# Kernel tuning notes

Hardware: AMD Instinct MI355X
Metric: run time of the kernel (lower is better)

## Reference

```python
import jax, jax.numpy as jnp
from jax import lax
import numpy as np

B = 16384
EPS = 1e-5


def conv2d(x, w, b, pad):
    # x: [N,C,H,W], w: [O,I,kh,kw]
    y = lax.conv_general_dilated(x, w, (1, 1), [(pad, pad), (pad, pad)],
                                 dimension_numbers=("NCHW", "OIHW", "NCHW"))
    return y + b[None, :, None, None]


def maxpool2(x):
    return lax.reduce_window(x, -jnp.inf, lax.max, (1, 1, 2, 2), (1, 1, 2, 2), "VALID")


def setup_inputs() -> dict:
    key = jax.random.key(0)
    ks = jax.random.split(key, 16)
    n = jax.random.normal
    return {
        "x": n(ks[0], (B, 1, 28, 28), dtype=jnp.float32),
        "conv1_w": n(ks[1], (8, 1, 3, 3), dtype=jnp.float32) * 0.2,
        "conv1_b": n(ks[2], (8,), dtype=jnp.float32) * 0.1,
        "conv2_w": n(ks[3], (16, 8, 3, 3), dtype=jnp.float32) * 0.1,
        "conv2_b": n(ks[4], (16,), dtype=jnp.float32) * 0.1,
        "s1_w": n(ks[5], (4, 2), dtype=jnp.float32) * 0.5,
        "s1_b": n(ks[6], (4,), dtype=jnp.float32) * 0.1,
        "s2_w": n(ks[7], (2, 4), dtype=jnp.float32) * 0.5,
        "s2_b": n(ks[8], (2,), dtype=jnp.float32) * 0.1,
        "filt_w": n(ks[9], (1, 1, 2, 2), dtype=jnp.float32) * 0.5,
        "filt_b": n(ks[10], (1,), dtype=jnp.float32) * 0.1,
        "fc1_w": n(ks[11], (64, 787), dtype=jnp.float32) * 0.03,
        "fc1_b": n(ks[12], (64,), dtype=jnp.float32) * 0.1,
        "fc2_w": n(ks[13], (4, 64), dtype=jnp.float32) * 0.1,
        "fc2_b": n(ks[14], (4,), dtype=jnp.float32) * 0.1,
        "bn_g": jnp.ones((4,), dtype=jnp.float32),
        "bn_b": jnp.zeros((4,), dtype=jnp.float32),
    }


def reference(x, conv1_w, conv1_b, conv2_w, conv2_b, s1_w, s1_b, s2_w, s2_b,
              filt_w, filt_b, fc1_w, fc1_b, fc2_w, fc2_b, bn_g, bn_b):
    bsz = x.shape[0]
    # feature extractor: conv3x3 -> relu -> maxpool2 (x2)
    f = maxpool2(jax.nn.relu(conv2d(x, conv1_w, conv1_b, 1)))        # [B,8,14,14]
    f = maxpool2(jax.nn.relu(conv2d(f, conv2_w, conv2_b, 1)))        # [B,16,7,7]
    flat = f.reshape(bsz, -1)                                        # [B,784]
    # sampler on first two features
    h = jnp.tanh(flat[:, :2] @ s1_w.T + s1_b)
    sampler_out = jax.nn.softmax(h @ s2_w.T + s2_b, axis=-1)         # [B,2]
    # conv filter: 2x2 stride-1 conv + sigmoid, mean over all patches
    logits = conv2d(x, filt_w, filt_b, 0)                            # [B,1,27,27]
    conv_out = jnp.mean(jax.nn.sigmoid(logits), axis=(1, 2, 3))[:, None]  # [B,1]
    combined = jnp.concatenate([flat, sampler_out, conv_out], axis=1)  # [B,787]
    out = jax.nn.relu(combined @ fc1_w.T + fc1_b) @ fc2_w.T + fc2_b    # [B,4]
    # BatchNorm1d, training mode (batch stats, biased variance)
    mu = jnp.mean(out, axis=0)
    var = jnp.var(out, axis=0)
    return (out - mu) * lax.rsqrt(var + EPS) * bn_g + bn_b
```

## Files before the change

### kernel.cpp

```cpp
#include <hip/hip_runtime.h>
#include <hip/hip_fp16.h>
#include <math.h>

#define NBATCH 16384
#define EPSV 1e-5f
#define IMGW 4

typedef short short8 __attribute__((ext_vector_type(8)));
typedef _Float16 half8_t __attribute__((ext_vector_type(8)));
typedef short short2v __attribute__((ext_vector_type(2)));
typedef float f32x4 __attribute__((ext_vector_type(4)));
union V8 { uint4 u; short8 s; };
union VH { uint4 u; half8_t h; };

__device__ __forceinline__ unsigned short f2bf(float f) {
    unsigned int x = __float_as_uint(f);
    return (unsigned short)((x + 0x7fffu + ((x >> 16) & 1u)) >> 16);
}
__device__ __forceinline__ unsigned short f2h(float f) {
    return __half_as_ushort(__float2half(f));
}
__device__ __forceinline__ __half2 u2h(unsigned int u) { return __builtin_bit_cast(__half2, u); }
__device__ __forceinline__ unsigned int h2u(__half2 h) { return __builtin_bit_cast(unsigned int, h); }

__global__ __launch_bounds__(256) void k_prep(
    const float* __restrict__ fc1w, const float* __restrict__ w2,
    const float* __restrict__ w1, const float* __restrict__ b1,
    unsigned short* __restrict__ wt, unsigned short* __restrict__ af16,
    unsigned int* __restrict__ w1h2, unsigned int* __restrict__ b1h2)
{
    int i = blockIdx.x * 256 + threadIdx.x;
    if (i < 51200) {
        int n = i / 800, k = i - n * 800;
        float v;
        if (k < 784) {
            int pos = k >> 4, oc = k & 15;
            v = fc1w[n * 787 + oc * 49 + pos];
        } else if (k < 787) {
            v = fc1w[n * 787 + k];
        } else {
            v = 0.f;
        }
        wt[i] = f2h(v);
    } else if (i < 52736) {
        int a = i - 51200;
        int slot = a >> 7, rem = a & 127, oc = rem >> 3, ic = rem & 7;
        float v = (slot < 9) ? w2[oc * 72 + ic * 9 + slot] : 0.f;
        af16[a] = f2h(v);
    } else if (i < 52808) {
        int k = i - 52736;
        unsigned int hb = f2h(w1[k]);
        w1h2[k] = hb | (hb << 16);
    } else if (i < 52816) {
        int k = i - 52808;
        unsigned int hb = f2h(b1[k]);
        b1h2[k] = hb | (hb << 16);
    }
}

#define SXS 15

__global__ __launch_bounds__(64, 4) void k_conv(
    const float* __restrict__ x,
    const float* __restrict__ s1w, const float* __restrict__ s1b,
    const float* __restrict__ s2w, const float* __restrict__ s2b,
    const float* __restrict__ fw, const float* __restrict__ fb,
    const float* __restrict__ b2,
    const unsigned short* __restrict__ Afg,
    const unsigned int* __restrict__ w1h2g,
    const unsigned int* __restrict__ b1h2g,
    unsigned short* __restrict__ comb)
{
    const int l = threadIdx.x;

    __shared__ unsigned int sxu[30 * SXS];
    __shared__ __align__(16) unsigned short sf1[16 * 136];

    for (int i = l; i < 30 * SXS; i += 64) sxu[i] = 0u;
    if (l < 60) {
        int R, C;
        if (l < 16)      { R = 0;      C = l; }
        else if (l < 32) { R = 15;     C = l - 16; }
        else if (l < 46) { R = l - 31; C = 0; }
        else             { R = l - 45; C = 15; }
        *reinterpret_cast<uint4*>(&sf1[R * 136 + C * 8]) = uint4{0u, 0u, 0u, 0u};
    }

    const __half2 fwh0 = __float2half2_rn(fw[0]);
    const __half2 fwh1 = __float2half2_rn(fw[1]);
    const __half2 fwh2 = __float2half2_rn(fw[2]);
    const __half2 fwh3 = __float2half2_rn(fw[3]);
    const __half2 fbh  = __float2half2_rn(fb[0]);
    float s1wv[8], s1bv[4], s2wv[8];
    #pragma unroll
    for (int k = 0; k < 8; ++k) s1wv[k] = s1w[k];
    #pragma unroll
    for (int k = 0; k < 4; ++k) s1bv[k] = s1b[k];
    #pragma unroll
    for (int k = 0; k < 8; ++k) s2wv[k] = s2w[k];
    const float s2b0 = s2b[0], s2b1 = s2b[1];

    const int n = l & 15, g = l >> 4;
    const int qr = n & 7;
    const int q = (qr < 7) ? qr : 6;
    const int dr = n >> 3;
    VH af[3];
    const unsigned short* ps[3];
    #pragma unroll
    for (int s = 0; s < 3; ++s) {
        const int slot = s * 4 + g;
        const int u = slot / 3, v = slot - 3 * (slot / 3);
        const int offs = (slot <= 8) ? (u * 136 + v * 8) : 0;
        ps[s] = sf1 + dr * 136 + 16 * q + offs;
        af[s].u = *reinterpret_cast<const uint4*>(Afg + ((slot * 16 + n) << 3));
    }
    float biasv[4];
    #pragma unroll
    for (int i = 0; i < 4; ++i) biasv[i] = b2[4 * g + i];

    int srow[7], sww[7];
    #pragma unroll
    for (int k = 0; k < 7; ++k) {
        int u0 = l + k * 64;
        srow[k] = u0 / 15;
        sww[k]  = u0 - srow[k] * 15;
    }

    const int b0 = blockIdx.x * IMGW;

    float xlo[7], xhi[7];
    {
        const float* xb = x + (size_t)b0 * 784;
        #pragma unroll
        for (int k = 0; k < 7; ++k) {
            const int u0 = l + k * 64;
            if (u0 < 420) {
                const float* base = xb + srow[k] * 28;
                xlo[k] = (sww[k] == 0)  ? 0.f : base[2 * sww[k] - 1];
                xhi[k] = (sww[k] == 14) ? 0.f : base[2 * sww[k]];
            }
        }
    }

    #pragma unroll
    for (int img = 0; img < IMGW; ++img) {
        const int b = b0 + img;
        unsigned short* crow = comb + (size_t)b * 800;

        #pragma unroll
        for (int k = 0; k < 7; ++k) {
            const int u0 = l + k * 64;
            if (u0 < 420)
                sxu[(srow[k] + 1) * SXS + sww[k]] = h2u(__floats2half2_rn(xlo[k], xhi[k]));
        }

        float ylo[7], yhi[7];
        if (img + 1 < IMGW) {
            const float* xb = x + (size_t)(b + 1) * 784;
            #pragma unroll
            for (int k = 0; k < 7; ++k) {
                const int u0 = l + k * 64;
                if (u0 < 420) {
                    const float* base = xb + srow[k] * 28;
                    ylo[k] = (sww[k] == 0)  ? 0.f : base[2 * sww[k] - 1];
                    yhi[k] = (sww[k] == 14) ? 0.f : base[2 * sww[k]];
                }
            }
        }

        if (l < 13) crow[787 + l] = 0;

        float fsum = 0.f;
        for (int u0 = l; u0 < 378; u0 += 64) {
            int r = u0 / 14, cp = u0 - (u0 / 14) * 14;
            unsigned int A1 = sxu[(r + 1) * SXS + cp], B1 = sxu[(r + 1) * SXS + cp + 1];
            unsigned int A2 = sxu[(r + 2) * SXS + cp], B2 = sxu[(r + 2) * SXS + cp + 1];
            __half2 al1 = u2h(__builtin_amdgcn_alignbit(B1, A1, 16));
            __half2 al2 = u2h(__builtin_amdgcn_alignbit(B2, A2, 16));
            __half2 acc = __hfma2(fwh0, al1,
                          __hfma2(fwh1, u2h(B1),
                          __hfma2(fwh2, al2,
                          __hfma2(fwh3, u2h(B2), fbh))));
            float2 f = __half22float2(acc);
            fsum += __frcp_rn(1.f + __expf(-f.x));
            if (cp < 13) fsum += __frcp_rn(1.f + __expf(-f.y));
        }
        #pragma unroll
        for (int off = 32; off > 0; off >>= 1)
            fsum += __shfl_xor(fsum, off, 64);

        for (int i = l; i < 196; i += 64) {
            const int p = i / 14, j = i - (i / 14) * 14;
            unsigned int A[4], B[4], M[4];
            #pragma unroll
            for (int u = 0; u < 4; ++u) {
                A[u] = sxu[(2 * p + u) * SXS + j];
                B[u] = sxu[(2 * p + u) * SXS + j + 1];
                M[u] = __builtin_amdgcn_alignbit(B[u], A[u], 16);
            }
            unsigned short outv[8];
            #pragma unroll
            for (int oc = 0; oc < 8; ++oc) {
                __half2 a0 = u2h(b1h2g[oc]), a1 = a0;
                #pragma unroll
                for (int u = 0; u < 3; ++u) {
                    #pragma unroll
                    for (int v = 0; v < 3; ++v) {
                        const __half2 wv = u2h(w1h2g[oc * 9 + u * 3 + v]);
                        const unsigned int p0 = (v == 0) ? A[u]     : ((v == 1) ? M[u]     : B[u]);
                        const unsigned int p1 = (v == 0) ? A[u + 1] : ((v == 1) ? M[u + 1] : B[u + 1]);
                        a0 = __hfma2(wv, u2h(p0), a0);
                        a1 = __hfma2(wv, u2h(p1), a1);
                    }
                }
                short2v s0 = __builtin_bit_cast(short2v, a0);
                short2v s1 = __builtin_bit_cast(short2v, a1);
                short2v mm = __builtin_elementwise_max(s0, s1);
                short m = mm[0] > mm[1] ? mm[0] : mm[1];
                if (m < 0) m = 0;
                outv[oc] = (unsigned short)m;
            }
            *reinterpret_cast<uint4*>(&sf1[(p + 1) * 136 + (j + 1) * 8]) =
                *reinterpret_cast<const uint4*>(outv);
        }

        float f0r = 0.f, f1r = 0.f;
        #pragma unroll
        for (int pp = 0; pp < 7; ++pp) {
            f32x4 acc0 = {0.f, 0.f, 0.f, 0.f}, acc1 = {0.f, 0.f, 0.f, 0.f};
            #pragma unroll
            for (int s = 0; s < 3; ++s) {
                VH c0, c1;
                c0.u = *reinterpret_cast<const uint4*>(ps[s] + pp * 272);
                c1.u = *reinterpret_cast<const uint4*>(ps[s] + pp * 272 + 8);
                acc0 = __builtin_amdgcn_mfma_f32_16x16x32_f16(af[s].h, c0.h, acc0, 0, 0, 0);
                acc1 = __builtin_amdgcn_mfma_f32_16x16x32_f16(af[s].h, c1.h, acc1, 0, 0, 0);
            }
            float vv[4];
            #pragma unroll
            for (int i = 0; i < 4; ++i) {
                float m = fmaxf(acc0[i], acc1[i]);
                m = fmaxf(m, __shfl_xor(m, 8, 64));
                vv[i] = fmaxf(m + biasv[i], 0.f);
            }
            if (pp == 0) {
                f0r = __shfl(vv[0], 0, 64);
                f1r = __shfl(vv[0], 1, 64);
            }
            if (n < 7) {
                uint2 pk;
                pk.x = (unsigned int)f2h(vv[0]) | ((unsigned int)f2h(vv[1]) << 16);
                pk.y = (unsigned int)f2h(vv[2]) | ((unsigned int)f2h(vv[3]) << 16);
                *reinterpret_cast<uint2*>(&crow[(pp * 7 + q) * 16 + g * 4]) = pk;
            }
        }

        if (l == 0) {
            crow[786] = f2h(fsum * (1.f / 729.f));
            float h[4];
            #pragma unroll
            for (int k = 0; k < 4; ++k) {
                float y = fmaf(f0r, s1wv[2 * k], fmaf(f1r, s1wv[2 * k + 1], s1bv[k]));
                float e = __expf(2.f * y);
                h[k] = (e - 1.f) * __frcp_rn(e + 1.f);
            }
            float l0 = s2b0, l1 = s2b1;
            #pragma unroll
            for (int k = 0; k < 4; ++k) {
                l0 = fmaf(h[k], s2wv[k], l0);
                l1 = fmaf(h[k], s2wv[4 + k], l1);
            }
            float mx = fmaxf(l0, l1);
            float e0 = __expf(l0 - mx), e1 = __expf(l1 - mx);
            float inv = __frcp_rn(e0 + e1);
            crow[784] = f2h(e0 * inv);
            crow[785] = f2h(e1 * inv);
        }

        if (img + 1 < IMGW) {
            #pragma unroll
            for (int k = 0; k < 7; ++k) { xlo[k] = ylo[k]; xhi[k] = yhi[k]; }
        }
    }
}

__global__ __launch_bounds__(256) void k_fc(
    const unsigned short* __restrict__ A,
    const unsigned short* __restrict__ Bw,
    const float* __restrict__ fc1b,
    const float* __restrict__ fc2w, const float* __restrict__ fc2b,
    float* __restrict__ out, float* __restrict__ part)
{
    __shared__ uint4 Asm[2][256];
    __shared__ uint4 Bsm[2][256];
    __shared__ float sh[64][68];
    __shared__ float sfc2[4][64];
    __shared__ float pacc[4][8];

    const int t = threadIdx.x;
    const int w = t >> 6, l = t & 63;
    const int blk = blockIdx.x;

    sfc2[t >> 6][t & 63] = fc2w[t];

    const int srow = t >> 2, skbp = t & 3;
    const int skbl = skbp ^ ((srow >> 1) & 3);
    const uint4* Ag = reinterpret_cast<const uint4*>(A) + ((size_t)blk * 64 + srow) * 100;
    const uint4* Bg = reinterpret_cast<const uint4*>(Bw) + (size_t)srow * 100;
    const int sidx = srow * 4 + skbp;

    const int arow = w * 16 + (l & 15);
    const int aidx = arow * 4 + ((l >> 4) ^ ((arow >> 1) & 3));
    int bidx[4];
    #pragma unroll
    for (int nf = 0; nf < 4; ++nf) {
        int nn = nf * 16 + (l & 15);
        bidx[nf] = nn * 4 + ((l >> 4) ^ ((nn >> 1) & 3));
    }

    f32x4 acc0 = {0.f, 0.f, 0.f, 0.f}, acc1 = acc0, acc2 = acc0, acc3 = acc0;

    Asm[0][sidx] = Ag[skbl];
    Bsm[0][sidx] = Bg[skbl];

    int buf = 0;
    for (int s = 0; s < 25; ++s) {
        __syncthreads();
        if (s < 24) {
            Asm[buf ^ 1][sidx] = Ag[(s + 1) * 4 + skbl];
            Bsm[buf ^ 1][sidx] = Bg[(s + 1) * 4 + skbl];
        }
        VH av; av.u = Asm[buf][aidx];
        VH b0; b0.u = Bsm[buf][bidx[0]];
        VH b1; b1.u = Bsm[buf][bidx[1]];
        VH b2; b2.u = Bsm[buf][bidx[2]];
        VH b3; b3.u = Bsm[buf][bidx[3]];
        acc0 = __builtin_amdgcn_mfma_f32_16x16x32_f16(av.h, b0.h, acc0, 0, 0, 0);
        acc1 = __builtin_amdgcn_mfma_f32_16x16x32_f16(av.h, b1.h, acc1, 0, 0, 0);
        acc2 = __builtin_amdgcn_mfma_f32_16x16x32_f16(av.h, b2.h, acc2, 0, 0, 0);
        acc3 = __builtin_amdgcn_mfma_f32_16x16x32_f16(av.h, b3.h, acc3, 0, 0, 0);
        buf ^= 1;
    }

    {
        const int c0 = l & 15, r0 = w * 16 + (l >> 4) * 4;
        float fb0 = fc1b[c0], fb1 = fc1b[16 + c0], fb2 = fc1b[32 + c0], fb3 = fc1b[48 + c0];
        #pragma unroll
        for (int r = 0; r < 4; ++r) {
            sh[r0 + r][c0]      = fmaxf(acc0[r] + fb0, 0.f);
            sh[r0 + r][16 + c0] = fmaxf(acc1[r] + fb1, 0.f);
            sh[r0 + r][32 + c0] = fmaxf(acc2[r] + fb2, 0.f);
            sh[r0 + r][48 + c0] = fmaxf(acc3[r] + fb3, 0.f);
        }
    }
    __syncthreads();

    {
        const int row = t >> 2, oo = t & 3;
        float s = fc2b[oo];
        #pragma unroll 8
        for (int o = 0; o < 64; ++o)
            s = fmaf(sh[row][o], sfc2[oo][o], s);
        out[((size_t)blk * 64 + row) * 4 + oo] = s;

        float rs = s, rq = s * s;
        #pragma unroll
        for (int off = 4; off < 64; off <<= 1) {
            rs += __shfl_xor(rs, off, 64);
            rq += __shfl_xor(rq, off, 64);
        }
        if (l < 4) pacc[w][l] = rs;
        else if (l < 8) pacc[w][l] = rq;
    }
    __syncthreads();
    if (t < 8)
        part[blk * 8 + t] = pacc[0][t] + pacc[1][t] + pacc[2][t] + pacc[3][t];
}

__global__ void k_bnfinal(const float* __restrict__ part,
                          const float* __restrict__ g, const float* __restrict__ bb,
                          float* __restrict__ ss, int nblocks)
{
    const int t = threadIdx.x;
    float s[8];
    #pragma unroll
    for (int i = 0; i < 8; ++i) s[i] = 0.f;
    for (int idx = t; idx < nblocks; idx += 64)
        #pragma unroll
        for (int i = 0; i < 8; ++i) s[i] += part[idx * 8 + i];
    #pragma unroll
    for (int i = 0; i < 8; ++i)
        #pragma unroll
        for (int off = 32; off > 0; off >>= 1)
            s[i] += __shfl_xor(s[i], off, 64);
    if (t == 0) {
        const float invB = 1.f / 16384.f;
        #pragma unroll
        for (int j = 0; j < 4; ++j) {
            float mu = s[j] * invB;
            float var = s[4 + j] * invB - mu * mu;
            float sc = g[j] * rsqrtf(var + EPSV);
            ss[j] = sc;
            ss[4 + j] = bb[j] - mu * sc;
        }
    }
}

__global__ __launch_bounds__(256) void k_bnapply(const float* __restrict__ ss,
                                                 float* __restrict__ out)
{
    const int row = blockIdx.x * 256 + threadIdx.x;
    float4 v = reinterpret_cast<float4*>(out)[row];
    v.x = fmaf(v.x, ss[0], ss[4]);
    v.y = fmaf(v.y, ss[1], ss[5]);
    v.z = fmaf(v.z, ss[2], ss[6]);
    v.w = fmaf(v.w, ss[3], ss[7]);
    reinterpret_cast<float4*>(out)[row] = v;
}

__global__ __launch_bounds__(256) void k_transpose_fb(const float* __restrict__ in,
                                                      float* __restrict__ out)
{
    int i = blockIdx.x * 256 + threadIdx.x;
    if (i < 787 * 64) {
        int k = i >> 6, o = i & 63;
        out[i] = in[o * 787 + k];
    }
}

#define SF1F(ic, r, c) sf1[(ic) * 324 + (r) * 20 + (c)]

__global__ __launch_bounds__(256) void k_fused_fb(
    const float* __restrict__ x,
    const float* __restrict__ w1, const float* __restrict__ b1,
    const float* __restrict__ w2, const float* __restrict__ b2,
    const float* __restrict__ s1w, const float* __restrict__ s1b,
    const float* __restrict__ s2w, const float* __restrict__ s2b,
    const float* __restrict__ fw, const float* __restrict__ fb,
    const float* __restrict__ wt, const float* __restrict__ fc1b,
    const float* __restrict__ fc2w, const float* __restrict__ fc2b,
    float* __restrict__ pre)
{
    const int b = blockIdx.x;
    const int t = threadIdx.x;

    __shared__ float sxA[30][20];
    __shared__ float sxB[30][20];
    __shared__ float sf1[8 * 324];
    __shared__ float scomb[788];
    __shared__ float sw1[72];
    __shared__ float sb1[8];
    __shared__ float sw2p[16 * 76];
    __shared__ float sb2[16];
    __shared__ float sh1p[4][64];
    __shared__ float sh1[64];
    __shared__ float sred[4];
    __shared__ float ssm[27];

    for (int i = t; i < 600; i += 256) { (&sxA[0][0])[i] = 0.f; (&sxB[0][0])[i] = 0.f; }
    for (int i = t; i < 8 * 324; i += 256) sf1[i] = 0.f;
    if (t < 72) sw1[t] = w1[t];
    if (t < 8) sb1[t] = b1[t];
    for (int i = t; i < 1152; i += 256) {
        int oc = i / 72, rem = i - oc * 72;
        sw2p[oc * 76 + rem] = w2[i];
    }
    if (t < 16) sb2[t] = b2[t];
    if (t < 8) ssm[t] = s1w[t];
    else if (t < 12) ssm[t] = s1b[t - 8];
    else if (t < 20) ssm[t] = s2w[t - 12];
    else if (t < 22) ssm[t] = s2b[t - 20];
    else if (t < 26) ssm[t] = fw[t - 22];
    else if (t == 26) ssm[t] = fb[0];
    __syncthreads();

    const float* xb = x + (size_t)b * 784;
    for (int i = t; i < 784; i += 256) {
        int r = i / 28, c = i - (i / 28) * 28;
        float v = xb[i];
        int pr = r + 1, pc = c + 1;
        if (pc <= 15) sxA[pr][pc] = v;
        if (pc >= 14) sxB[pr][pc - 14] = v;
    }
    __syncthreads();

    {
        const float fw00 = ssm[22], fw01 = ssm[23], fw10 = ssm[24], fw11 = ssm[25];
        const float fbv = ssm[26];
        float fsum = 0.f;
        for (int i = t; i < 729; i += 256) {
            int r = i / 27, c = i - (i / 27) * 27;
            float x00, x01, x10, x11;
            if (c <= 13) {
                x00 = sxA[r + 1][c + 1]; x01 = sxA[r + 1][c + 2];
                x10 = sxA[r + 2][c + 1]; x11 = sxA[r + 2][c + 2];
            } else {
                int cb = c - 14;
                x00 = sxB[r + 1][cb + 1]; x01 = sxB[r + 1][cb + 2];
                x10 = sxB[r + 2][cb + 1]; x11 = sxB[r + 2][cb + 2];
            }
            float v = fbv;
            v = fmaf(x00, fw00, v); v = fmaf(x01, fw01, v);
            v = fmaf(x10, fw10, v); v = fmaf(x11, fw11, v);
            fsum += 1.f / (1.f + expf(-v));
        }
        #pragma unroll
        for (int off = 32; off > 0; off >>= 1)
            fsum += __shfl_xor(fsum, off, 64);
        if ((t & 63) == 0) sred[t >> 6] = fsum;
    }

    {
        const int half = t >> 7;
        const int id = t & 127;
        if (id < 112) {
            const int p = id >> 3, oc = id & 7;
            const float* base = half ? &sxB[0][0] : &sxA[0][0];
            float X[4][16];
            #pragma unroll
            for (int u = 0; u < 4; ++u) {
                const float4* rp = reinterpret_cast<const float4*>(base + (2 * p + u) * 20);
                float4 a = rp[0], bb4 = rp[1], c4 = rp[2], d4 = rp[3];
                X[u][0] = a.x;  X[u][1] = a.y;  X[u][2] = a.z;  X[u][3] = a.w;
                X[u][4] = bb4.x; X[u][5] = bb4.y; X[u][6] = bb4.z; X[u][7] = bb4.w;
                X[u][8] = c4.x;  X[u][9] = c4.y;  X[u][10] = c4.z; X[u][11] = c4.w;
                X[u][12] = d4.x; X[u][13] = d4.y; X[u][14] = d4.z; X[u][15] = d4.w;
            }
            float W[9];
            #pragma unroll
            for (int k = 0; k < 9; ++k) W[k] = sw1[oc * 9 + k];
            const float bias = sb1[oc];
            const int j0 = half * 7;
            #pragma unroll
            for (int jj = 0; jj < 7; ++jj) {
                float m = 0.f;
                #pragma unroll
                for (int dr = 0; dr < 2; ++dr)
                    #pragma unroll
                    for (int dc = 0; dc < 2; ++dc) {
                        float acc = bias;
                        #pragma unroll
                        for (int u = 0; u < 3; ++u)
                            #pragma unroll
                            for (int v = 0; v < 3; ++v)
                                acc = fmaf(X[dr + u][2 * jj + dc + v], W[u * 3 + v], acc);
                        m = fmaxf(m, acc);
                    }
                SF1F(oc, p + 1, j0 + jj + 1) = m;
            }
        }
    }
    __syncthreads();

    if (t < 112) {
        const int p = t >> 4, oc = t & 15;
        const float bias = sb2[oc];
        float acc[7][4];
        #pragma unroll
        for (int jj = 0; jj < 7; ++jj)
            #pragma unroll
            for (int s = 0; s < 4; ++s) acc[jj][s] = bias;
        for (int ic = 0; ic < 8; ++ic) {
            float X[4][16];
            #pragma unroll
            for (int u = 0; u < 4; ++u) {
                const float4* rp = reinterpret_cast<const float4*>(&SF1F(ic, 2 * p + u, 0));
                float4 a = rp[0], bb4 = rp[1], c4 = rp[2], d4 = rp[3];
                X[u][0] = a.x;  X[u][1] = a.y;  X[u][2] = a.z;  X[u][3] = a.w;
                X[u][4] = bb4.x; X[u][5] = bb4.y; X[u][6] = bb4.z; X[u][7] = bb4.w;
                X[u][8] = c4.x;  X[u][9] = c4.y;  X[u][10] = c4.z; X[u][11] = c4.w;
                X[u][12] = d4.x; X[u][13] = d4.y; X[u][14] = d4.z; X[u][15] = d4.w;
            }
            float W[9];
            #pragma unroll
            for (int k = 0; k < 9; ++k) W[k] = sw2p[oc * 76 + ic * 9 + k];
            #pragma unroll
            for (int jj = 0; jj < 7; ++jj)
                #pragma unroll
                for (int dr = 0; dr < 2; ++dr)
                    #pragma unroll
                    for (int dc = 0; dc < 2; ++dc)
                        #pragma unroll
                        for (int u = 0; u < 3; ++u)
                            #pragma unroll
                            for (int v = 0; v < 3; ++v)
                                acc[jj][dr * 2 + dc] =
                                    fmaf(X[dr + u][2 * jj + dc + v], W[u * 3 + v], acc[jj][dr * 2 + dc]);
        }
        #pragma unroll
        for (int jj = 0; jj < 7; ++jj) {
            float m = fmaxf(fmaxf(acc[jj][0], acc[jj][1]), fmaxf(acc[jj][2], acc[jj][3]));
            scomb[oc * 49 + p * 7 + jj] = fmaxf(m, 0.f);
        }
    }
    __syncthreads();

    if (t == 0) {
        scomb[786] = (sred[0] + sred[1] + sred[2] + sred[3]) * (1.f / 729.f);
        float f0 = scomb[0], f1 = scomb[1];
        float h[4];
        #pragma unroll
        for (int k = 0; k < 4; ++k)
            h[k] = tanhf(fmaf(f0, ssm[k * 2], fmaf(f1, ssm[k * 2 + 1], ssm[8 + k])));
        float l0 = ssm[20], l1 = ssm[21];
        #pragma unroll
        for (int k = 0; k < 4; ++k) {
            l0 = fmaf(h[k], ssm[12 + k], l0);
            l1 = fmaf(h[k], ssm[16 + k], l1);
        }
        float mx = fmaxf(l0, l1);
        float e0 = expf(l0 - mx), e1 = expf(l1 - mx);
        float inv = 1.f / (e0 + e1);
        scomb[784] = e0 * inv;
        scomb[785] = e1 * inv;
    }
    __syncthreads();

    {
        const int o = t & 63, w = t >> 6;
        const int k0 = w * 197;
        const int k1 = (w == 3) ? 787 : k0 + 197;
        const float* wp = wt + (size_t)k0 * 64 + o;
        float acc = 0.f;
        #pragma unroll 4
        for (int k = k0; k < k1; ++k) {
            acc = fmaf(scomb[k], *wp, acc);
            wp += 64;
        }
        sh1p[w][o] = acc;
    }
    __syncthreads();
    if (t < 64)
        sh1[t] = fmaxf(sh1p[0][t] + sh1p[1][t] + sh1p[2][t] + sh1p[3][t] + fc1b[t], 0.f);
    __syncthreads();

    {
        const int oo = t >> 6, lane = t & 63;
        float v = sh1[lane] * fc2w[oo * 64 + lane];
        #pragma unroll
        for (int off = 32; off > 0; off >>= 1)
            v += __shfl_xor(v, off, 64);
        if (lane == 0) pre[(size_t)b * 4 + oo] = v + fc2b[oo];
    }
}

__global__ __launch_bounds__(256) void k_bnstat_fb(const float* __restrict__ pre,
                                                   float* __restrict__ part)
{
    const int t = threadIdx.x;
    const int row = blockIdx.x * 256 + t;
    float4 v = reinterpret_cast<const float4*>(pre)[row];
    float s0 = v.x, s1 = v.y, s2 = v.z, s3 = v.w;
    float q0 = v.x * v.x, q1 = v.y * v.y, q2 = v.z * v.z, q3 = v.w * v.w;
    #pragma unroll
    for (int off = 32; off > 0; off >>= 1) {
        s0 += __shfl_xor(s0, off, 64);
        s1 += __shfl_xor(s1, off, 64);
        s2 += __shfl_xor(s2, off, 64);
        s3 += __shfl_xor(s3, off, 64);
        q0 += __shfl_xor(q0, off, 64);
        q1 += __shfl_xor(q1, off, 64);
        q2 += __shfl_xor(q2, off, 64);
        q3 += __shfl_xor(q3, off, 64);
    }
    __shared__ float acc[4][8];
    if ((t & 63) == 0) {
        int w = t >> 6;
        acc[w][0] = s0; acc[w][1] = s1; acc[w][2] = s2; acc[w][3] = s3;
        acc[w][4] = q0; acc[w][5] = q1; acc[w][6] = q2; acc[w][7] = q3;
    }
    __syncthreads();
    if (t < 8)
        part[blockIdx.x * 8 + t] = acc[0][t] + acc[1][t] + acc[2][t] + acc[3][t];
}

extern "C" void kernel_launch(void* const* d_in, const int* in_sizes, int n_in,
                              void* d_out, int out_size, void* d_ws, size_t ws_size,
                              hipStream_t stream)
{
    const float* x    = (const float*)d_in[0];
    const float* w1   = (const float*)d_in[1];
    const float* b1   = (const float*)d_in[2];
    const float* w2   = (const float*)d_in[3];
    const float* b2   = (const float*)d_in[4];
    const float* s1w  = (const float*)d_in[5];
    const float* s1b  = (const float*)d_in[6];
    const float* s2w  = (const float*)d_in[7];
    const float* s2b  = (const float*)d_in[8];
    const float* fw   = (const float*)d_in[9];
    const float* fb   = (const float*)d_in[10];
    const float* fc1w = (const float*)d_in[11];
    const float* fc1b = (const float*)d_in[12];
    const float* fc2w = (const float*)d_in[13];
    const float* fc2b = (const float*)d_in[14];
    const float* bng  = (const float*)d_in[15];
    const float* bnb  = (const float*)d_in[16];

    float* out = (float*)d_out;

    const size_t COMB_BYTES = (size_t)NBATCH * 800 * 2;
    const size_t WT_BYTES   = 64 * 800 * 2;
    const size_t AF16_BYTES = 1536 * 2;
    const size_t W1H2_BYTES = 72 * 4;
    const size_t B1H2_BYTES = 8 * 4;
    const size_t PART_BYTES = 256 * 8 * 4;
    const size_t NEED = COMB_BYTES + WT_BYTES + AF16_BYTES + W1H2_BYTES +
                        B1H2_BYTES + PART_BYTES + 32;

    if (ws_size >= NEED) {
        char* p = (char*)d_ws;
        unsigned short* comb = (unsigned short*)p;                     p += COMB_BYTES;
        unsigned short* wtbf = (unsigned short*)p;                     p += WT_BYTES;
        unsigned short* af16 = (unsigned short*)p;                     p += AF16_BYTES;
        unsigned int*   w1h2 = (unsigned int*)p;                       p += W1H2_BYTES;
        unsigned int*   b1h2 = (unsigned int*)p;                       p += B1H2_BYTES;
        float*          part = (float*)p;                              p += PART_BYTES;
        float*          ss   = (float*)p;

        k_prep<<<207, 256, 0, stream>>>(fc1w, w2, w1, b1, wtbf, af16, w1h2, b1h2);
        k_conv<<<NBATCH / IMGW, 64, 0, stream>>>(x, s1w, s1b, s2w, s2b, fw, fb, b2,
                                                 af16, w1h2, b1h2, comb);
        k_fc<<<256, 256, 0, stream>>>(comb, wtbf, fc1b, fc2w, fc2b, out, part);
        k_bnfinal<<<1, 64, 0, stream>>>(part, bng, bnb, ss, 256);
        k_bnapply<<<64, 256, 0, stream>>>(ss, out);
    } else {
        float* part = (float*)d_ws;
        float* ss   = part + 512;
        float* wt   = ss + 8;

        k_transpose_fb<<<197, 256, 0, stream>>>(fc1w, wt);
        k_fused_fb<<<NBATCH, 256, 0, stream>>>(x, w1, b1, w2, b2, s1w, s1b, s2w, s2b,
                                               fw, fb, wt, fc1b, fc2w, fc2b, out);
        k_bnstat_fb<<<64, 256, 0, stream>>>(out, part);
        k_bnfinal<<<1, 64, 0, stream>>>(part, bng, bnb, ss, 64);
        k_bnapply<<<64, 256, 0, stream>>>(ss, out);
    }
}
```

Baseline: 95.64 us.

## Process one image per conv block and fold BN finalize into apply kernel

The conv kernel now handles one image per 64-thread block instead of four, dropping the software prefetch of the next image. Its occupancy hint rises from 4 to 8 blocks per unit and the grid grows fourfold. The separate single-block BN finalize kernel is removed: every block of the apply kernel reduces the 256 partial sums itself and computes scale and shift, saving one launch. In exchange, weight setup and loads are repeated per image, the overlap of the next image's global load with compute is lost, and the partial-sum reduction is done redundantly in every apply block.

New measurement: 87.10 us (median of 2 runs). 1.1x faster.

```diff
diff --git a/kernel.cpp b/kernel.cpp
--- a/kernel.cpp
+++ b/kernel.cpp
@@ -4,7 +4,6 @@
 
 #define NBATCH 16384
 #define EPSV 1e-5f
-#define IMGW 4
 
 typedef short short8 __attribute__((ext_vector_type(8)));
 typedef _Float16 half8_t __attribute__((ext_vector_type(8)));
@@ -60,7 +59,7 @@
 
 #define SXS 15
 
-__global__ __launch_bounds__(64, 4) void k_conv(
+__global__ __launch_bounds__(64, 8) void k_conv(
     const float* __restrict__ x,
     const float* __restrict__ s1w, const float* __restrict__ s1b,
     const float* __restrict__ s2w, const float* __restrict__ s2b,
@@ -91,14 +90,6 @@
     const __half2 fwh2 = __float2half2_rn(fw[2]);
     const __half2 fwh3 = __float2half2_rn(fw[3]);
     const __half2 fbh  = __float2half2_rn(fb[0]);
-    float s1wv[8], s1bv[4], s2wv[8];
-    #pragma unroll
-    for (int k = 0; k < 8; ++k) s1wv[k] = s1w[k];
-    #pragma unroll
-    for (int k = 0; k < 4; ++k) s1bv[k] = s1b[k];
-    #pragma unroll
-    for (int k = 0; k < 8; ++k) s2wv[k] = s2w[k];
-    const float s2b0 = s2b[0], s2b1 = s2b[1];
 
     const int n = l & 15, g = l >> 4;
     const int qr = n & 7;
@@ -126,161 +117,133 @@
         sww[k]  = u0 - srow[k] * 15;
     }
 
-    const int b0 = blockIdx.x * IMGW;
+    const int b = blockIdx.x;
+    const float* xb = x + (size_t)b * 784;
+    unsigned short* crow = comb + (size_t)b * 800;
+
+    if (l < 13) crow[787 + l] = 0;
 
     float xlo[7], xhi[7];
-    {
-        const float* xb = x + (size_t)b0 * 784;
-        #pragma unroll
-        for (int k = 0; k < 7; ++k) {
-            const int u0 = l + k * 64;
-            if (u0 < 420) {
-                const float* base = xb + srow[k] * 28;
-                xlo[k] = (sww[k] == 0)  ? 0.f : base[2 * sww[k] - 1];
-                xhi[k] = (sww[k] == 14) ? 0.f : base[2 * sww[k]];
-            }
-        }
-    }
-
-    #pragma unroll
-    for (int img = 0; img < IMGW; ++img) {
-        const int b = b0 + img;
-        unsigned short* crow = comb + (size_t)b * 800;
-
-        #pragma unroll
-        for (int k = 0; k < 7; ++k) {
-            const int u0 = l + k * 64;
-            if (u0 < 420)
-                sxu[(srow[k] + 1) * SXS + sww[k]] = h2u(__floats2half2_rn(xlo[k], xhi[k]));
-        }
-
-        float ylo[7], yhi[7];
-        if (img + 1 < IMGW) {
-            const float* xb = x + (size_t)(b + 1) * 784;
+    #pragma unroll
+    for (int k = 0; k < 7; ++k) {
+        const int u0 = l + k * 64;
+        if (u0 < 420) {
+            const float* base = xb + srow[k] * 28;
+            xlo[k] = (sww[k] == 0)  ? 0.f : base[2 * sww[k] - 1];
+            xhi[k] = (sww[k] == 14) ? 0.f : base[2 * sww[k]];
+        }
+    }
+    #pragma unroll
+    for (int k = 0; k < 7; ++k) {
+        const int u0 = l + k * 64;
+        if (u0 < 420)
+            sxu[(srow[k] + 1) * SXS + sww[k]] = h2u(__floats2half2_rn(xlo[k], xhi[k]));
+    }
+
+    float fsum = 0.f;
+    for (int u0 = l; u0 < 378; u0 += 64) {
+        int r = u0 / 14, cp = u0 - (u0 / 14) * 14;
+        unsigned int A1 = sxu[(r + 1) * SXS + cp], B1 = sxu[(r + 1) * SXS + cp + 1];
+        unsigned int A2 = sxu[(r + 2) * SXS + cp], B2 = sxu[(r + 2) * SXS + cp + 1];
+        __half2 al1 = u2h(__builtin_amdgcn_alignbit(B1, A1, 16));
+        __half2 al2 = u2h(__builtin_amdgcn_alignbit(B2, A2, 16));
+        __half2 acc = __hfma2(fwh0, al1,
+                      __hfma2(fwh1, u2h(B1),
+                      __hfma2(fwh2, al2,
+                      __hfma2(fwh3, u2h(B2), fbh))));
+        float2 f = __half22float2(acc);
+        fsum += __frcp_rn(1.f + __expf(-f.x));
+        if (cp < 13) fsum += __frcp_rn(1.f + __expf(-f.y));
+    }
+    #pragma unroll
+    for (int off = 32; off > 0; off >>= 1)
+        fsum += __shfl_xor(fsum, off, 64);
+
+    for (int i = l; i < 196; i += 64) {
+        const int p = i / 14, j = i - (i / 14) * 14;
+        unsigned int A[4], B[4], M[4];
+        #pragma unroll
+        for (int u = 0; u < 4; ++u) {
+            A[u] = sxu[(2 * p + u) * SXS + j];
+            B[u] = sxu[(2 * p + u) * SXS + j + 1];
+            M[u] = __builtin_amdgcn_alignbit(B[u], A[u], 16);
+        }
+        unsigned short outv[8];
+        #pragma unroll
+        for (int oc = 0; oc < 8; ++oc) {
+            __half2 a0 = u2h(b1h2g[oc]), a1 = a0;
             #pragma unroll
-            for (int k = 0; k < 7; ++k) {
-                const int u0 = l + k * 64;
-                if (u0 < 420) {
-                    const float* base = xb + srow[k] * 28;
-                    ylo[k] = (sww[k] == 0)  ? 0.f : base[2 * sww[k] - 1];
-                    yhi[k] = (sww[k] == 14) ? 0.f : base[2 * sww[k]];
+            for (int u = 0; u < 3; ++u) {
+                #pragma unroll
+                for (int v = 0; v < 3; ++v) {
+                    const __half2 wv = u2h(w1h2g[oc * 9 + u * 3 + v]);
+                    const unsigned int p0 = (v == 0) ? A[u]     : ((v == 1) ? M[u]     : B[u]);
+                    const unsigned int p1 = (v == 0) ? A[u + 1] : ((v == 1) ? M[u + 1] : B[u + 1]);
+                    a0 = __hfma2(wv, u2h(p0), a0);
+                    a1 = __hfma2(wv, u2h(p1), a1);
                 }
             }
-        }
-
-        if (l < 13) crow[787 + l] = 0;
-
-        float fsum = 0.f;
-        for (int u0 = l; u0 < 378; u0 += 64) {
-            int r = u0 / 14, cp = u0 - (u0 / 14) * 14;
-            unsigned int A1 = sxu[(r + 1) * SXS + cp], B1 = sxu[(r + 1) * SXS + cp + 1];
-            unsigned int A2 = sxu[(r + 2) * SXS + cp], B2 = sxu[(r + 2) * SXS + cp + 1];
-            __half2 al1 = u2h(__builtin_amdgcn_alignbit(B1, A1, 16));
-            __half2 al2 = u2h(__builtin_amdgcn_alignbit(B2, A2, 16));
-            __half2 acc = __hfma2(fwh0, al1,
-                          __hfma2(fwh1, u2h(B1),
-                          __hfma2(fwh2, al2,
-                          __hfma2(fwh3, u2h(B2), fbh))));
-            float2 f = __half22float2(acc);
-            fsum += __frcp_rn(1.f + __expf(-f.x));
-            if (cp < 13) fsum += __frcp_rn(1.f + __expf(-f.y));
-        }
-        #pragma unroll
-        for (int off = 32; off > 0; off >>= 1)
-            fsum += __shfl_xor(fsum, off, 64);
-
-        for (int i = l; i < 196; i += 64) {
-            const int p = i / 14, j = i - (i / 14) * 14;
-            unsigned int A[4], B[4], M[4];
-            #pragma unroll
-            for (int u = 0; u < 4; ++u) {
-                A[u] = sxu[(2 * p + u) * SXS + j];
-                B[u] = sxu[(2 * p + u) * SXS + j + 1];
-                M[u] = __builtin_amdgcn_alignbit(B[u], A[u], 16);
-            }
-            unsigned short outv[8];
-            #pragma unroll
-            for (int oc = 0; oc < 8; ++oc) {
-                __half2 a0 = u2h(b1h2g[oc]), a1 = a0;
-                #pragma unroll
-                for (int u = 0; u < 3; ++u) {
-                    #pragma unroll
-                    for (int v = 0; v < 3; ++v) {
-                        const __half2 wv = u2h(w1h2g[oc * 9 + u * 3 + v]);
-                        const unsigned int p0 = (v == 0) ? A[u]     : ((v == 1) ? M[u]     : B[u]);
-                        const unsigned int p1 = (v == 0) ? A[u + 1] : ((v == 1) ? M[u + 1] : B[u + 1]);
-                        a0 = __hfma2(wv, u2h(p0), a0);
-                        a1 = __hfma2(wv, u2h(p1), a1);
-                    }
-                }
-                short2v s0 = __builtin_bit_cast(short2v, a0);
-                short2v s1 = __builtin_bit_cast(short2v, a1);
-                short2v mm = __builtin_elementwise_max(s0, s1);
-                short m = mm[0] > mm[1] ? mm[0] : mm[1];
-                if (m < 0) m = 0;
-                outv[oc] = (unsigned short)m;
-            }
-            *reinterpret_cast<uint4*>(&sf1[(p + 1) * 136 + (j + 1) * 8]) =
-                *reinterpret_cast<const uint4*>(outv);
-        }
-
-        float f0r = 0.f, f1r = 0.f;
-        #pragma unroll
-        for (int pp = 0; pp < 7; ++pp) {
-            f32x4 acc0 = {0.f, 0.f, 0.f, 0.f}, acc1 = {0.f, 0.f, 0.f, 0.f};
-            #pragma unroll
-            for (int s = 0; s < 3; ++s) {
-                VH c0, c1;
-                c0.u = *reinterpret_cast<const uint4*>(ps[s] + pp * 272);
-                c1.u = *reinterpret_cast<const uint4*>(ps[s] + pp * 272 + 8);
-                acc0 = __builtin_amdgcn_mfma_f32_16x16x32_f16(af[s].h, c0.h, acc0, 0, 0, 0);
-                acc1 = __builtin_amdgcn_mfma_f32_16x16x32_f16(af[s].h, c1.h, acc1, 0, 0, 0);
-            }
-            float vv[4];
-            #pragma unroll
-            for (int i = 0; i < 4; ++i) {
-                float m = fmaxf(acc0[i], acc1[i]);
-                m = fmaxf(m, __shfl_xor(m, 8, 64));
-                vv[i] = fmaxf(m + biasv[i], 0.f);
-            }
-            if (pp == 0) {
-                f0r = __shfl(vv[0], 0, 64);
-                f1r = __shfl(vv[0], 1, 64);
-            }
-            if (n < 7) {
-                uint2 pk;
-                pk.x = (unsigned int)f2h(vv[0]) | ((unsigned int)f2h(vv[1]) << 16);
-                pk.y = (unsigned int)f2h(vv[2]) | ((unsigned int)f2h(vv[3]) << 16);
-                *reinterpret_cast<uint2*>(&crow[(pp * 7 + q) * 16 + g * 4]) = pk;
-            }
-        }
-
-        if (l == 0) {
-            crow[786] = f2h(fsum * (1.f / 729.f));
-            float h[4];
-            #pragma unroll
-            for (int k = 0; k < 4; ++k) {
-                float y = fmaf(f0r, s1wv[2 * k], fmaf(f1r, s1wv[2 * k + 1], s1bv[k]));
-                float e = __expf(2.f * y);
-                h[k] = (e - 1.f) * __frcp_rn(e + 1.f);
-            }
-            float l0 = s2b0, l1 = s2b1;
-            #pragma unroll
-            for (int k = 0; k < 4; ++k) {
-                l0 = fmaf(h[k], s2wv[k], l0);
-                l1 = fmaf(h[k], s2wv[4 + k], l1);
-            }
-            float mx = fmaxf(l0, l1);
-            float e0 = __expf(l0 - mx), e1 = __expf(l1 - mx);
-            float inv = __frcp_rn(e0 + e1);
-            crow[784] = f2h(e0 * inv);
-            crow[785] = f2h(e1 * inv);
-        }
-
-        if (img + 1 < IMGW) {
-            #pragma unroll
-            for (int k = 0; k < 7; ++k) { xlo[k] = ylo[k]; xhi[k] = yhi[k]; }
-        }
+            short2v s0 = __builtin_bit_cast(short2v, a0);
+            short2v s1 = __builtin_bit_cast(short2v, a1);
+            short2v mm = __builtin_elementwise_max(s0, s1);
+            short m = mm[0] > mm[1] ? mm[0] : mm[1];
+            if (m < 0) m = 0;
+            outv[oc] = (unsigned short)m;
+        }
+        *reinterpret_cast<uint4*>(&sf1[(p + 1) * 136 + (j + 1) * 8]) =
+            *reinterpret_cast<const uint4*>(outv);
+    }
+
+    float f0r = 0.f, f1r = 0.f;
+    for (int pp = 0; pp < 7; ++pp) {
+        f32x4 acc0 = {0.f, 0.f, 0.f, 0.f}, acc1 = {0.f, 0.f, 0.f, 0.f};
+        #pragma unroll
+        for (int s = 0; s < 3; ++s) {
+            VH c0, c1;
+            c0.u = *reinterpret_cast<const uint4*>(ps[s] + pp * 272);
+            c1.u = *reinterpret_cast<const uint4*>(ps[s] + pp * 272 + 8);
+            acc0 = __builtin_amdgcn_mfma_f32_16x16x32_f16(af[s].h, c0.h, acc0, 0, 0, 0);
+            acc1 = __builtin_amdgcn_mfma_f32_16x16x32_f16(af[s].h, c1.h, acc1, 0, 0, 0);
+        }
+        float vv[4];
+        #pragma unroll
+        for (int i = 0; i < 4; ++i) {
+            float m = fmaxf(acc0[i], acc1[i]);
+            m = fmaxf(m, __shfl_xor(m, 8, 64));
+            vv[i] = fmaxf(m + biasv[i], 0.f);
+        }
+        if (pp == 0) {
+            f0r = __shfl(vv[0], 0, 64);
+            f1r = __shfl(vv[0], 1, 64);
+        }
+        if (n < 7) {
+            uint2 pk;
+            pk.x = (unsigned int)f2h(vv[0]) | ((unsigned int)f2h(vv[1]) << 16);
+            pk.y = (unsigned int)f2h(vv[2]) | ((unsigned int)f2h(vv[3]) << 16);
+            *reinterpret_cast<uint2*>(&crow[(pp * 7 + q) * 16 + g * 4]) = pk;
+        }
+    }
+
+    if (l == 0) {
+        crow[786] = f2h(fsum * (1.f / 729.f));
+        float h[4];
+        #pragma unroll
+        for (int k = 0; k < 4; ++k) {
+            float y = fmaf(f0r, s1w[2 * k], fmaf(f1r, s1w[2 * k + 1], s1b[k]));
+            float e = __expf(2.f * y);
+            h[k] = (e - 1.f) * __frcp_rn(e + 1.f);
+        }
+        float l0 = s2b[0], l1 = s2b[1];
+        #pragma unroll
+        for (int k = 0; k < 4; ++k) {
+            l0 = fmaf(h[k], s2w[k], l0);
+            l1 = fmaf(h[k], s2w[4 + k], l1);
+        }
+        float mx = fmaxf(l0, l1);
+        float e0 = __expf(l0 - mx), e1 = __expf(l1 - mx);
+        float inv = __frcp_rn(e0 + e1);
+        crow[784] = f2h(e0 * inv);
+        crow[785] = f2h(e1 * inv);
     }
 }
 
@@ -377,44 +340,49 @@
         part[blk * 8 + t] = pacc[0][t] + pacc[1][t] + pacc[2][t] + pacc[3][t];
 }
 
-__global__ void k_bnfinal(const float* __restrict__ part,
-                          const float* __restrict__ g, const float* __restrict__ bb,
-                          float* __restrict__ ss, int nblocks)
+__global__ __launch_bounds__(256) void k_bnapply(const float* __restrict__ part,
+                                                 const float* __restrict__ g,
+                                                 const float* __restrict__ bb,
+                                                 float* __restrict__ out)
 {
     const int t = threadIdx.x;
+    __shared__ float red[4][8];
+
     float s[8];
     #pragma unroll
-    for (int i = 0; i < 8; ++i) s[i] = 0.f;
-    for (int idx = t; idx < nblocks; idx += 64)
-        #pragma unroll
-        for (int i = 0; i < 8; ++i) s[i] += part[idx * 8 + i];
+    for (int i = 0; i < 8; ++i) s[i] = part[t * 8 + i];
     #pragma unroll
     for (int i = 0; i < 8; ++i)
         #pragma unroll
         for (int off = 32; off > 0; off >>= 1)
             s[i] += __shfl_xor(s[i], off, 64);
-    if (t == 0) {
+    if ((t & 63) == 0) {
+        #pragma unroll
+        for (int i = 0; i < 8; ++i) red[t >> 6][i] = s[i];
+    }
+    __syncthreads();
+
+    float sc[4], sh[4];
+    {
         const float invB = 1.f / 16384.f;
         #pragma unroll
         for (int j = 0; j < 4; ++j) {
-            float mu = s[j] * invB;
-            float var = s[4 + j] * invB - mu * mu;
-            float sc = g[j] * rsqrtf(var + EPSV);
-            ss[j] = sc;
-            ss[4 + j] = bb[j] - mu * sc;
-        }
-    }
-}
-
-__global__ __launch_bounds__(256) void k_bnapply(const float* __restrict__ ss,
-                                                 float* __restrict__ out)
-{
-    const int row = blockIdx.x * 256 + threadIdx.x;
+            float tot  = red[0][j] + red[1][j] + red[2][j] + red[3][j];
+            float totq = red[0][4 + j] + red[1][4 + j] + red[2][4 + j] + red[3][4 + j];
+            float mu = tot * invB;
+            float var = totq * invB - mu * mu;
+            float s2 = g[j] * rsqrtf(var + EPSV);
+            sc[j] = s2;
+            sh[j] = bb[j] - mu * s2;
+        }
+    }
+
+    const int row = blockIdx.x * 256 + t;
     float4 v = reinterpret_cast<float4*>(out)[row];
-    v.x = fmaf(v.x, ss[0], ss[4]);
-    v.y = fmaf(v.y, ss[1], ss[5]);
-    v.z = fmaf(v.z, ss[2], ss[6]);
-    v.w = fmaf(v.w, ss[3], ss[7]);
+    v.x = fmaf(v.x, sc[0], sh[0]);
+    v.y = fmaf(v.y, sc[1], sh[1]);
+    v.z = fmaf(v.z, sc[2], sh[2]);
+    v.w = fmaf(v.w, sc[3], sh[3]);
     reinterpret_cast<float4*>(out)[row] = v;
 }
 
@@ -674,6 +642,47 @@
         part[blockIdx.x * 8 + t] = acc[0][t] + acc[1][t] + acc[2][t] + acc[3][t];
 }
 
+__global__ void k_bnfinal_fb(const float* __restrict__ part,
+                             const float* __restrict__ g, const float* __restrict__ bb,
+                             float* __restrict__ ss, int nblocks)
+{
+    const int t = threadIdx.x;
+    float s[8];
+    #pragma unroll
+    for (int i = 0; i < 8; ++i) s[i] = 0.f;
+    for (int idx = t; idx < nblocks; idx += 64)
+        #pragma unroll
+        for (int i = 0; i < 8; ++i) s[i] += part[idx * 8 + i];
+    #pragma unroll
+    for (int i = 0; i < 8; ++i)
+        #pragma unroll
+        for (int off = 32; off > 0; off >>= 1)
+            s[i] += __shfl_xor(s[i], off, 64);
+    if (t == 0) {
+        const float invB = 1.f / 16384.f;
+        #pragma unroll
+        for (int j = 0; j < 4; ++j) {
+            float mu = s[j] * invB;
+            float var = s[4 + j] * invB - mu * mu;
+            float sc = g[j] * rsqrtf(var + EPSV);
+            ss[j] = sc;
+            ss[4 + j] = bb[j] - mu * sc;
+        }
+    }
+}
+
+__global__ __launch_bounds__(256) void k_bnapply_fb(const float* __restrict__ ss,
+                                                    float* __restrict__ out)
+{
+    const int row = blockIdx.x * 256 + threadIdx.x;
+    float4 v = reinterpret_cast<float4*>(out)[row];
+    v.x = fmaf(v.x, ss[0], ss[4]);
+    v.y = fmaf(v.y, ss[1], ss[5]);
+    v.z = fmaf(v.z, ss[2], ss[6]);
+    v.w = fmaf(v.w, ss[3], ss[7]);
+    reinterpret_cast<float4*>(out)[row] = v;
+}
+
 extern "C" void kernel_launch(void* const* d_in, const int* in_sizes, int n_in,
                               void* d_out, int out_size, void* d_ws, size_t ws_size,
                               hipStream_t stream)
@@ -714,15 +723,13 @@
         unsigned short* af16 = (unsigned short*)p;                     p += AF16_BYTES;
         unsigned int*   w1h2 = (unsigned int*)p;                       p += W1H2_BYTES;
         unsigned int*   b1h2 = (unsigned int*)p;                       p += B1H2_BYTES;
-        float*          part = (float*)p;                              p += PART_BYTES;
-        float*          ss   = (float*)p;
+        float*          part = (float*)p;
 
         k_prep<<<207, 256, 0, stream>>>(fc1w, w2, w1, b1, wtbf, af16, w1h2, b1h2);
-        k_conv<<<NBATCH / IMGW, 64, 0, stream>>>(x, s1w, s1b, s2w, s2b, fw, fb, b2,
-                                                 af16, w1h2, b1h2, comb);
+        k_conv<<<NBATCH, 64, 0, stream>>>(x, s1w, s1b, s2w, s2b, fw, fb, b2,
+                                          af16, w1h2, b1h2, comb);
         k_fc<<<256, 256, 0, stream>>>(comb, wtbf, fc1b, fc2w, fc2b, out, part);
-        k_bnfinal<<<1, 64, 0, stream>>>(part, bng, bnb, ss, 256);
-        k_bnapply<<<64, 256, 0, stream>>>(ss, out);
+        k_bnapply<<<64, 256, 0, stream>>>(part, bng, bnb, out);
     } else {
         float* part = (float*)d_ws;
         float* ss   = part + 512;
@@ -732,7 +739,7 @@
         k_fused_fb<<<NBATCH, 256, 0, stream>>>(x, w1, b1, w2, b2, s1w, s1b, s2w, s2b,
                                                fw, fb, wt, fc1b, fc2w, fc2b, out);
         k_bnstat_fb<<<64, 256, 0, stream>>>(out, part);
-        k_bnfinal<<<1, 64, 0, stream>>>(part, bng, bnb, ss, 64);
-        k_bnapply<<<64, 256, 0, stream>>>(ss, out);
-    }
-}
+        k_bnfinal_fb<<<1, 64, 0, stream>>>(part, bng, bnb, ss, 64);
+        k_bnapply_fb<<<64, 256, 0, stream>>>(ss, out);
+    }
+}
```
